# Kernel optimization log

Measured on AMD Instinct MI355X. Metric: run time of the kernel, lower is better.

The kernel has to match this reference:

```python
import jax, jax.numpy as jnp
import numpy as np
from jax import lax

K = 3
ALPHA = 2000.0
TAU = 0.001
MAX_ITER = 100
EPS = 1e-7


def setup_inputs() -> dict:
    key = jax.random.key(0)
    x = jax.random.normal(key, (8, 2048, 32), dtype=jnp.float32)
    return {"x": x}


def _vmd(x):
    B, L, D = x.shape
    # shifted frequency grid, identical across B and D
    f = jnp.fft.fftshift(jnp.fft.fftfreq(L)).astype(x.dtype)          # [L]
    f_bld = f[None, :, None]                                           # [1,L,1]
    # nonnegative-frequency mask; torch code boolean-masks f_shifted >= 0,
    # which is uniform over B and D, so it is a weighted sum over L here
    pos = (f >= 0).astype(x.dtype)[None, None, :, None]                # [1,1,L,1]
    x_hat = jnp.fft.fftshift(jnp.fft.fft(x, axis=1), axes=1)          # [B,L,D] complex

    def step(carry, _):
        u, omega, lam = carry  # u:[B,K,L,D], omega:[B,K,D], lam:[B,L,D]
        # Gauss-Seidel mode updates (each mode sees already-updated others)
        for k_idx in range(K):
            sum_other = jnp.sum(u, axis=1) - u[:, k_idx]               # [B,L,D]
            sum_other_hat = jnp.fft.fftshift(jnp.fft.fft(sum_other, axis=1), axes=1)
            num = x_hat - sum_other_hat + lam * 0.5                    # lam added in freq domain, as in source
            den = 1.0 + 2.0 * ALPHA * (f_bld - omega[:, k_idx][:, None, :]) ** 2
            u_k = jnp.real(jnp.fft.ifft(jnp.fft.ifftshift(num / den, axes=1), axis=1))
            u = u.at[:, k_idx].set(u_k)
        # center-frequency update over nonnegative shifted frequencies
        u_hat = jnp.fft.fftshift(jnp.fft.fft(u, axis=2), axes=2)       # [B,K,L,D]
        p = (u_hat.real ** 2 + u_hat.imag ** 2) * pos                  # |u_hat|^2 masked
        omega = jnp.sum(f[None, None, :, None] * p, axis=2) / (jnp.sum(p, axis=2) + EPS)  # [B,K,D]
        # dual ascent on lambda
        lam = lam + TAU * (x - jnp.sum(u, axis=1))
        return (u, omega, lam), None

    u0 = jnp.zeros((B, K, L, D), x.dtype)
    om0 = jnp.zeros((B, K, D), x.dtype)
    lam0 = jnp.zeros((B, L, D), x.dtype)
    (u, omega, _), _ = lax.scan(jax.checkpoint(step), (u0, om0, lam0), None, length=MAX_ITER)

    # sort modes per batch element by mean center frequency
    order = jnp.argsort(jnp.mean(omega, axis=2), axis=1)               # [B,K]
    u_sorted = jnp.take_along_axis(u, order[:, :, None, None], axis=1)
    return u_sorted[:, 0], u_sorted[:, 1], u_sorted[:, 2]


def reference(x):
    return _vmd(x)
```

## Files before the change

kernel.cpp:

```cpp
#include <hip/hip_runtime.h>

#define PD(i) ((i) + ((i) >> 5))
#define BLD 524288

__device__ __forceinline__ float2 cadd(float2 a, float2 b){ return make_float2(a.x+b.x, a.y+b.y); }
__device__ __forceinline__ float2 csub(float2 a, float2 b){ return make_float2(a.x-b.x, a.y-b.y); }
__device__ __forceinline__ float2 cmul(float2 a, float2 b){ return make_float2(a.x*b.x - a.y*b.y, a.x*b.y + a.y*b.x); }
__device__ __forceinline__ float2 cmuli(float2 a, float s){ return make_float2(-s*a.y, s*a.x); }

template<int CTRL, int RM>
__device__ __forceinline__ float dpp_add(float x){
  int r = __builtin_amdgcn_update_dpp(0, __float_as_int(x), CTRL, RM, 0xf, true);
  return x + __int_as_float(r);
}
__device__ __forceinline__ float wave_sum64(float x){
  x = dpp_add<0x111,0xf>(x);
  x = dpp_add<0x112,0xf>(x);
  x = dpp_add<0x114,0xf>(x);
  x = dpp_add<0x118,0xf>(x);
  x = dpp_add<0x142,0xa>(x);
  x = dpp_add<0x143,0xc>(x);
  return x;
}

template<int SGN>
__device__ __forceinline__ void dft8(float2 a[8]) {
  const float sgn = (float)SGN;
  const float C8 = 0.70710678118654752440f;
  float2 e0=a[0], e1=a[2], e2=a[4], e3=a[6];
  float2 o0=a[1], o1=a[3], o2=a[5], o3=a[7];
  float2 t0=cadd(e0,e2), t1=csub(e0,e2), t2=cadd(e1,e3), t3=csub(e1,e3);
  float2 E0=cadd(t0,t2), E2=csub(t0,t2);
  float2 t3i=cmuli(t3,sgn);
  float2 E1=cadd(t1,t3i), E3=csub(t1,t3i);
  float2 s0=cadd(o0,o2), s1=csub(o0,o2), s2=cadd(o1,o3), s3=csub(o1,o3);
  float2 O0=cadd(s0,s2), O2=csub(s0,s2);
  float2 s3i=cmuli(s3,sgn);
  float2 O1=cadd(s1,s3i), O3=csub(s1,s3i);
  float2 w1o = make_float2(C8*(O1.x - sgn*O1.y), C8*(O1.y + sgn*O1.x));
  float2 w2o = cmuli(O2, sgn);
  float2 w3o = make_float2(-C8*(O3.x + sgn*O3.y), C8*(sgn*O3.x - O3.y));
  a[0]=cadd(E0,O0); a[4]=csub(E0,O0);
  a[1]=cadd(E1,w1o); a[5]=csub(E1,w1o);
  a[2]=cadd(E2,w2o); a[6]=csub(E2,w2o);
  a[3]=cadd(E3,w3o); a[7]=csub(E3,w3o);
}

template<int SGN>
__device__ void fft2048(float2* bufA, float2* bufB, const float2* twd, int tid)
{
  const float sgn = (float)SGN;
  {
    float2 a[8];
    #pragma unroll
    for (int j=0;j<8;j++) a[j] = bufA[PD(tid + 256*j)];
    dft8<SGN>(a);
    float2 tw = twd[tid];
    float2 w1 = make_float2(tw.x, sgn*tw.y), wj = w1;
    #pragma unroll
    for (int j=1;j<8;j++){ a[j] = cmul(a[j], wj); wj = cmul(wj, w1); }
    #pragma unroll
    for (int j=0;j<8;j++) bufB[PD(8*tid + j)] = a[j];
  }
  __syncthreads();
  {
    float2 a[8];
    #pragma unroll
    for (int j=0;j<8;j++) a[j] = bufB[PD(tid + 256*j)];
    dft8<SGN>(a);
    int p = tid >> 3, q = tid & 7;
    float2 tw = twd[p << 3];
    float2 w1 = make_float2(tw.x, sgn*tw.y), wj = w1;
    #pragma unroll
    for (int j=1;j<8;j++){ a[j] = cmul(a[j], wj); wj = cmul(wj, w1); }
    int base = q + (p << 6);
    #pragma unroll
    for (int j=0;j<8;j++) bufA[PD(base + (j<<3))] = a[j];
  }
  __syncthreads();
  {
    float2 a[8];
    #pragma unroll
    for (int j=0;j<8;j++) a[j] = bufA[PD(tid + 256*j)];
    dft8<SGN>(a);
    int p = tid >> 6, q = tid & 63;
    float2 tw = twd[p << 6];
    float2 w1 = make_float2(tw.x, sgn*tw.y), wj = w1;
    #pragma unroll
    for (int j=1;j<8;j++){ a[j] = cmul(a[j], wj); wj = cmul(wj, w1); }
    int base = q + (p << 9);
    #pragma unroll
    for (int j=0;j<8;j++) bufB[PD(base + (j<<6))] = a[j];
  }
  __syncthreads();
  {
    #pragma unroll
    for (int h=0; h<2; h++){
      int q = tid + (h<<8);
      float2 b0 = bufB[PD(q)], b1 = bufB[PD(q+512)], b2 = bufB[PD(q+1024)], b3 = bufB[PD(q+1536)];
      float2 t0=cadd(b0,b2), t1=csub(b0,b2), t2=cadd(b1,b3), t3=csub(b1,b3);
      float2 t3i=cmuli(t3,sgn);
      bufA[PD(q)]      = cadd(t0,t2);
      bufA[PD(q+512)]  = cadd(t1,t3i);
      bufA[PD(q+1024)] = csub(t0,t2);
      bufA[PD(q+1536)] = csub(t1,t3i);
    }
  }
  __syncthreads();
}

__device__ __forceinline__ void dft4p(float2 a[4]){
  float2 t0=cadd(a[0],a[2]), t1=csub(a[0],a[2]), t2=cadd(a[1],a[3]), t3=csub(a[1],a[3]);
  float2 t3i = make_float2(-t3.y, t3.x);
  a[0]=cadd(t0,t2); a[2]=csub(t0,t2);
  a[1]=cadd(t1,t3i); a[3]=csub(t1,t3i);
}

template<bool TRANSP>
__global__ __launch_bounds__(256, 1) void vmd_main(const float* __restrict__ xg,
                                                   float* __restrict__ uout,
                                                   float* __restrict__ omout)
{
  __shared__ float2 sbufA[2112];
  __shared__ float2 sbufB[2112];
  __shared__ float2 stwd[1024];
  __shared__ float  sred[24];

  const int tid = threadIdx.x;
  const int blk = blockIdx.x;
  const int b = blk >> 5;
  const int d = blk & 31;
  const float inv2048 = 1.0f/2048.0f;

  for (int j = tid; j < 1024; j += 256) {
    double th = 3.14159265358979323846 * (double)j / 1024.0;
    stwd[j] = make_float2((float)cos(th), (float)sin(th));
  }

  int idxs[8];
  float fl[4], fh[4];
  #pragma unroll
  for (int c = 0; c < 4; c++) {
    int iL = 4*tid + c;
    idxs[c]   = iL;
    idxs[c+4] = (iL == 0) ? 1024 : (2048 - iL);
    fl[c] = (float)(idxs[c]   - 1024) * inv2048;
    fh[c] = (float)(idxs[c+4] - 1024) * inv2048;
  }
  int sI[8];
  #pragma unroll
  for (int e = 0; e < 8; e++) sI[e] = PD(idxs[e]);

  float xv[8];
  #pragma unroll
  for (int e = 0; e < 8; e++) xv[e] = xg[(b*2048 + idxs[e])*32 + d];

  #pragma unroll
  for (int e = 0; e < 8; e++) {
    float v = (idxs[e] & 1) ? -xv[e] : xv[e];
    sbufA[sI[e]] = make_float2(v, 0.0f);
  }
  __syncthreads();
  fft2048<-1>(sbufA, sbufB, stwd, tid);
  float2 X[8];
  #pragma unroll
  for (int e = 0; e < 8; e++) X[e] = sbufA[sI[e]];

  int rd[4]; float2 wq[4];
  #pragma unroll
  for (int j = 0; j < 4; j++) { int q = tid + 256*j; rd[j] = PD(q); wq[j] = stwd[q]; }
  const int pw0 = PD(4*tid);
  float2 c1w1 = stwd[2*tid];
  float2 c1w2 = cmul(c1w1,c1w1), c1w3 = cmul(c1w2,c1w1);
  float2 s4w1 = stwd[8*(tid>>2)];
  float2 s4w2 = cmul(s4w1,s4w1), s4w3 = cmul(s4w2,s4w1);
  float2 s16w1 = stwd[32*(tid>>4)];
  float2 s16w2 = cmul(s16w1,s16w1), s16w3 = cmul(s16w2,s16w1);
  float2 s64w1 = stwd[128*(tid>>6)];
  float2 s64w2 = cmul(s64w1,s64w1), s64w3 = cmul(s64w2,s64w1);
  int w4i[4], w16i[4], w64i[4];
  { int base = (tid & 3) + ((tid>>2)<<4);
    #pragma unroll
    for (int j=0;j<4;j++) w4i[j]  = PD(base + (j<<2)); }
  { int base = (tid & 15) + ((tid>>4)<<6);
    #pragma unroll
    for (int j=0;j<4;j++) w16i[j] = PD(base + (j<<4)); }
  { int base = (tid & 63) + ((tid>>6)<<8);
    #pragma unroll
    for (int j=0;j<4;j++) w64i[j] = PD(base + (j<<6)); }
  const int zi0 = PD(2*tid), zi1 = PD(2*tid+1);
  const int zi2 = PD((tid==0) ? 512 : (1024 - 2*tid));
  const int zi3 = PD(1023 - 2*tid), zi4 = PD(1022 - 2*tid);

  auto herm = [&]() {
    {
      float2 C[4];
      #pragma unroll
      for (int j=0;j<4;j++){
        float2 lo = sbufB[rd[j]];
        float2 hi = sbufB[rd[j] + 1056];
        float2 Av = cadd(lo,hi), Bv = csub(lo,hi);
        float2 WB = cmul(wq[j], Bv);
        C[j] = make_float2(Av.x - WB.y, Av.y + WB.x);
      }
      dft4p(C);
      C[1]=cmul(C[1],c1w1); C[2]=cmul(C[2],c1w2); C[3]=cmul(C[3],c1w3);
      sbufA[pw0]   = C[0];
      sbufA[pw0+1] = C[1];
      sbufA[pw0+2] = C[2];
      sbufA[pw0+3] = C[3];
    }
    __syncthreads();
    {
      float2 a[4];
      #pragma unroll
      for (int j=0;j<4;j++) a[j] = sbufA[rd[j]];
      dft4p(a);
      a[1]=cmul(a[1],s4w1); a[2]=cmul(a[2],s4w2); a[3]=cmul(a[3],s4w3);
      #pragma unroll
      for (int j=0;j<4;j++) sbufB[w4i[j]] = a[j];
    }
    __syncthreads();
    {
      float2 a[4];
      #pragma unroll
      for (int j=0;j<4;j++) a[j] = sbufB[rd[j]];
      dft4p(a);
      a[1]=cmul(a[1],s16w1); a[2]=cmul(a[2],s16w2); a[3]=cmul(a[3],s16w3);
      #pragma unroll
      for (int j=0;j<4;j++) sbufA[w16i[j]] = a[j];
    }
    __syncthreads();
    {
      float2 a[4];
      #pragma unroll
      for (int j=0;j<4;j++) a[j] = sbufA[rd[j]];
      dft4p(a);
      a[1]=cmul(a[1],s64w1); a[2]=cmul(a[2],s64w2); a[3]=cmul(a[3],s64w3);
      #pragma unroll
      for (int j=0;j<4;j++) sbufB[w64i[j]] = a[j];
    }
    __syncthreads();
    {
      float2 a[4];
      #pragma unroll
      for (int j=0;j<4;j++) a[j] = sbufB[rd[j]];
      dft4p(a);
      #pragma unroll
      for (int j=0;j<4;j++) sbufA[rd[j]] = a[j];
    }
    __syncthreads();
  };

  float2 U[3][8];
  float2 S[8];
  float lam2[8];
  #pragma unroll
  for (int e = 0; e < 8; e++) {
    S[e] = make_float2(0.f, 0.f); lam2[e] = 0.f;
    #pragma unroll
    for (int k = 0; k < 3; k++) U[k][e] = make_float2(0.f, 0.f);
  }
  float om[3] = {0.f, 0.f, 0.f};
  const int wv = tid >> 6, ln = tid & 63;

  for (int iter = 0; iter < 100; iter++) {
    float xl[8];
    #pragma unroll
    for (int e = 0; e < 8; e++) xl[e] = X[e].x + lam2[e];

    float sf[3], sp[3];
    #pragma unroll
    for (int k = 0; k < 3; k++) {
      sf[k] = 0.f; sp[k] = 0.f;
      #pragma unroll
      for (int c = 0; c < 4; c++) {
        float2 numl = make_float2(xl[c]     - S[c].x   + U[k][c].x,
                                  X[c].y    - S[c].y   + U[k][c].y);
        float2 numh = make_float2(xl[c+4]   - S[c+4].x + U[k][c+4].x,
                                  X[c+4].y  - S[c+4].y + U[k][c+4].y);
        float dl = fl[c] - om[k], dh = fh[c] - om[k];
        float rl = __builtin_amdgcn_rcpf(fmaf(4000.0f*dl, dl, 1.0f));
        float rh = __builtin_amdgcn_rcpf(fmaf(4000.0f*dh, dh, 1.0f));
        float2 Vl = make_float2(numl.x*rl, numl.y*rl);
        float2 Vh = make_float2(numh.x*rh, numh.y*rh);
        float2 Ul, Uh;
        if (tid == 0 && c == 0) {
          Ul = make_float2(Vl.x, 0.f);
          Uh = make_float2(Vh.x, 0.f);
        } else {
          Ul = make_float2(0.5f*(Vl.x + Vh.x), 0.5f*(Vl.y - Vh.y));
          Uh = make_float2(Ul.x, -Ul.y);
        }
        S[c].x   += Ul.x - U[k][c].x;   S[c].y   += Ul.y - U[k][c].y;
        S[c+4].x += Uh.x - U[k][c+4].x; S[c+4].y += Uh.y - U[k][c+4].y;
        U[k][c] = Ul; U[k][c+4] = Uh;
        float pw = Uh.x*Uh.x + Uh.y*Uh.y;
        sf[k] = fmaf(fh[c], pw, sf[k]);
        sp[k] += pw;
      }
    }

    #pragma unroll
    for (int e = 0; e < 8; e++) sbufB[sI[e]] = S[e];

    #pragma unroll
    for (int k = 0; k < 3; k++) { sf[k] = wave_sum64(sf[k]); sp[k] = wave_sum64(sp[k]); }
    if (ln == 63) {
      #pragma unroll
      for (int k = 0; k < 3; k++) { sred[wv*6 + k] = sf[k]; sred[wv*6 + 3 + k] = sp[k]; }
    }
    __syncthreads();

    #pragma unroll
    for (int k = 0; k < 3; k++) {
      float a = sred[k] + sred[6+k] + sred[12+k] + sred[18+k];
      float p = sred[3+k] + sred[9+k] + sred[15+k] + sred[21+k];
      om[k] = a * __builtin_amdgcn_rcpf(p + 1e-7f);
    }

    herm();

    {
      float2 z0 = sbufA[zi0];
      float2 z1 = sbufA[zi1];
      float2 h0 = sbufA[zi2];
      float2 h1 = sbufA[zi3];
      float2 h2 = sbufA[zi4];
      float g[8];
      g[0]=z0.x; g[1]=z0.y; g[2]=z1.x; g[3]=z1.y;
      g[4]=h0.x; g[5]=h1.y; g[6]=h1.x; g[7]=h2.y;
      #pragma unroll
      for (int e = 0; e < 8; e++) {
        float sv = g[e] * inv2048;
        if (e & 1) sv = -sv;
        lam2[e] = fmaf(0.0005f, xv[e] - sv, lam2[e]);
      }
    }
  }

  #pragma unroll
  for (int k = 0; k < 3; k++) {
    #pragma unroll
    for (int e = 0; e < 8; e++) sbufB[sI[e]] = U[k][e];
    __syncthreads();
    herm();
    {
      float2 z0 = sbufA[zi0];
      float2 z1 = sbufA[zi1];
      float2 h0 = sbufA[zi2];
      float2 h1 = sbufA[zi3];
      float2 h2 = sbufA[zi4];
      float g[8];
      g[0]=z0.x; g[1]=z0.y; g[2]=z1.x; g[3]=z1.y;
      g[4]=h0.x; g[5]=h1.y; g[6]=h1.x; g[7]=h2.y;
      #pragma unroll
      for (int e = 0; e < 8; e++) {
        float uv = g[e] * inv2048;
        if (e & 1) uv = -uv;
        if (TRANSP) uout[(((size_t)k*8 + b)*32 + d)*2048 + idxs[e]] = uv;
        else        uout[(size_t)k*BLD + ((size_t)b*2048 + idxs[e])*32 + d] = uv;
      }
    }
  }
  if (tid == 0) {
    omout[(b*3 + 0)*32 + d] = om[0];
    omout[(b*3 + 1)*32 + d] = om[1];
    omout[(b*3 + 2)*32 + d] = om[2];
  }
}

__device__ __forceinline__ void order3(const float* sm, int* sord){
  float v0=sm[0], v1=sm[1], v2=sm[2];
  int j0=0,j1=1,j2=2;
  if (v1<v0){float tv=v0;v0=v1;v1=tv;int ti=j0;j0=j1;j1=ti;}
  if (v2<v1){float tv=v1;v1=v2;v2=tv;int ti=j1;j1=j2;j2=ti;}
  if (v1<v0){float tv=v0;v0=v1;v1=tv;int ti=j0;j0=j1;j1=ti;}
  sord[0]=j0; sord[1]=j1; sord[2]=j2;
}

__global__ __launch_bounds__(256) void vmd_permute(const float* __restrict__ wsu,
                                                   const float* __restrict__ omout,
                                                   float* __restrict__ out)
{
  __shared__ float tile[32][33];
  __shared__ float sm[3];
  __shared__ int sord[3];
  int bid = blockIdx.x;
  int lt = bid & 63;
  int b = (bid >> 6) & 7;
  int kpos = bid >> 9;
  int tid = threadIdx.x;
  if (tid < 3) {
    float s = 0.f;
    for (int dd = 0; dd < 32; dd++) s += omout[(b*3 + tid)*32 + dd];
    sm[tid] = s;
  }
  __syncthreads();
  if (tid == 0) order3(sm, sord);
  __syncthreads();
  int ks = sord[kpos];
  int tr = tid >> 5, tc = tid & 31;
  for (int it = 0; it < 4; it++) {
    int dd = tr + it*8;
    tile[dd][tc] = wsu[(((size_t)ks*8 + b)*32 + dd)*2048 + lt*32 + tc];
  }
  __syncthreads();
  for (int it = 0; it < 4; it++) {
    int ll = tr + it*8;
    out[(size_t)kpos*BLD + ((size_t)b*2048 + lt*32 + ll)*32 + tc] = tile[tc][ll];
  }
}

__global__ void vmd_inplace(float* __restrict__ out, const float* __restrict__ omout)
{
  __shared__ float sm[3];
  __shared__ int sord[3];
  int r = blockIdx.x * 256 + threadIdx.x;
  int b = r >> 16;
  if (threadIdx.x < 3) {
    float s = 0.f;
    for (int dd = 0; dd < 32; dd++) s += omout[(b*3 + threadIdx.x)*32 + dd];
    sm[threadIdx.x] = s;
  }
  __syncthreads();
  if (threadIdx.x == 0) order3(sm, sord);
  __syncthreads();
  int o0 = sord[0], o1 = sord[1], o2 = sord[2];
  float v0 = out[(size_t)o0*BLD + r];
  float v1 = out[(size_t)o1*BLD + r];
  float v2 = out[(size_t)o2*BLD + r];
  out[r] = v0;
  out[(size_t)BLD + r] = v1;
  out[(size_t)2*BLD + r] = v2;
}

extern "C" void kernel_launch(void* const* d_in, const int* in_sizes, int n_in,
                              void* d_out, int out_size, void* d_ws, size_t ws_size,
                              hipStream_t stream)
{
  const float* x = (const float*)d_in[0];
  float* out = (float*)d_out;
  const size_t NU = (size_t)3 * BLD;
  size_t need = NU*4 + 768*4;
  if (ws_size >= need) {
    float* wsu  = (float*)d_ws;
    float* wsom = wsu + NU;
    vmd_main<true><<<256, 256, 0, stream>>>(x, wsu, wsom);
    vmd_permute<<<1536, 256, 0, stream>>>(wsu, wsom, out);
  } else {
    float* wsom = (float*)d_ws;
    vmd_main<false><<<256, 256, 0, stream>>>(x, out, wsom);
    vmd_inplace<<<2048, 256, 0, stream>>>(out, wsom);
  }
}
```

Before: 313.2 us.

## Replace shared-memory radix-4 inverse FFT stages with in-wave lane-exchange butterflies

The per-iteration Hermitian inverse FFT used five shared-memory radix-4 passes separated by block barriers. It is replaced by one shared-memory radix-4 pass, followed by six radix-2 stages done inside each wave with ds_bpermute, ds_swizzle and DPP exchanges, and a final 4-way combine read from shared memory. This cuts block-wide barriers per iteration from about five to one or two. The mode update also keeps only half of the spectrum in registers by exploiting conjugate symmetry. The cost is more complex indexing and twiddle setup, extra cross-lane traffic, and some risk of numerical or index errors.

Result: faster. 302.7 us (-3.4%).

```diff
diff --git a/kernel.cpp b/kernel.cpp
--- a/kernel.cpp
+++ b/kernel.cpp
@@ -21,6 +21,24 @@
   x = dpp_add<0x142,0xa>(x);
   x = dpp_add<0x143,0xc>(x);
   return x;
+}
+
+__device__ __forceinline__ float2 exbp(int addr, float2 v){
+  return make_float2(
+    __int_as_float(__builtin_amdgcn_ds_bpermute(addr, __float_as_int(v.x))),
+    __int_as_float(__builtin_amdgcn_ds_bpermute(addr, __float_as_int(v.y))));
+}
+template<int PAT>
+__device__ __forceinline__ float2 exswz(float2 v){
+  return make_float2(
+    __int_as_float(__builtin_amdgcn_ds_swizzle(__float_as_int(v.x), PAT)),
+    __int_as_float(__builtin_amdgcn_ds_swizzle(__float_as_int(v.y), PAT)));
+}
+template<int CTRL>
+__device__ __forceinline__ float2 exdpp(float2 v){
+  return make_float2(
+    __int_as_float(__builtin_amdgcn_update_dpp(0, __float_as_int(v.x), CTRL, 0xF, 0xF, true)),
+    __int_as_float(__builtin_amdgcn_update_dpp(0, __float_as_int(v.y), CTRL, 0xF, 0xF, true)));
 }
 
 template<int SGN>
@@ -126,30 +144,31 @@
   __shared__ float2 stwd[1024];
   __shared__ float  sred[24];
 
-  const int tid = threadIdx.x;
+  float2* sS  = sbufB;
+  float2* sTY = sbufA;
+
+  const int t = threadIdx.x;
+  const int lane = t & 63;
+  const int w = t >> 6;
   const int blk = blockIdx.x;
   const int b = blk >> 5;
   const int d = blk & 31;
   const float inv2048 = 1.0f/2048.0f;
 
-  for (int j = tid; j < 1024; j += 256) {
+  for (int j = t; j < 1024; j += 256) {
     double th = 3.14159265358979323846 * (double)j / 1024.0;
     stwd[j] = make_float2((float)cos(th), (float)sin(th));
   }
 
   int idxs[8];
-  float fl[4], fh[4];
+  float fl[4];
   #pragma unroll
   for (int c = 0; c < 4; c++) {
-    int iL = 4*tid + c;
+    int iL = 4*t + c;
     idxs[c]   = iL;
     idxs[c+4] = (iL == 0) ? 1024 : (2048 - iL);
-    fl[c] = (float)(idxs[c]   - 1024) * inv2048;
-    fh[c] = (float)(idxs[c+4] - 1024) * inv2048;
-  }
-  int sI[8];
-  #pragma unroll
-  for (int e = 0; e < 8; e++) sI[e] = PD(idxs[e]);
+    fl[c] = (float)(iL - 1024) * inv2048;
+  }
 
   float xv[8];
   #pragma unroll
@@ -158,157 +177,191 @@
   #pragma unroll
   for (int e = 0; e < 8; e++) {
     float v = (idxs[e] & 1) ? -xv[e] : xv[e];
-    sbufA[sI[e]] = make_float2(v, 0.0f);
-  }
-  __syncthreads();
-  fft2048<-1>(sbufA, sbufB, stwd, tid);
-  float2 X[8];
-  #pragma unroll
-  for (int e = 0; e < 8; e++) X[e] = sbufA[sI[e]];
-
-  int rd[4]; float2 wq[4];
-  #pragma unroll
-  for (int j = 0; j < 4; j++) { int q = tid + 256*j; rd[j] = PD(q); wq[j] = stwd[q]; }
-  const int pw0 = PD(4*tid);
-  float2 c1w1 = stwd[2*tid];
-  float2 c1w2 = cmul(c1w1,c1w1), c1w3 = cmul(c1w2,c1w1);
-  float2 s4w1 = stwd[8*(tid>>2)];
-  float2 s4w2 = cmul(s4w1,s4w1), s4w3 = cmul(s4w2,s4w1);
-  float2 s16w1 = stwd[32*(tid>>4)];
-  float2 s16w2 = cmul(s16w1,s16w1), s16w3 = cmul(s16w2,s16w1);
-  float2 s64w1 = stwd[128*(tid>>6)];
-  float2 s64w2 = cmul(s64w1,s64w1), s64w3 = cmul(s64w2,s64w1);
-  int w4i[4], w16i[4], w64i[4];
-  { int base = (tid & 3) + ((tid>>2)<<4);
-    #pragma unroll
-    for (int j=0;j<4;j++) w4i[j]  = PD(base + (j<<2)); }
-  { int base = (tid & 15) + ((tid>>4)<<6);
-    #pragma unroll
-    for (int j=0;j<4;j++) w16i[j] = PD(base + (j<<4)); }
-  { int base = (tid & 63) + ((tid>>6)<<8);
-    #pragma unroll
-    for (int j=0;j<4;j++) w64i[j] = PD(base + (j<<6)); }
-  const int zi0 = PD(2*tid), zi1 = PD(2*tid+1);
-  const int zi2 = PD((tid==0) ? 512 : (1024 - 2*tid));
-  const int zi3 = PD(1023 - 2*tid), zi4 = PD(1022 - 2*tid);
-
-  auto herm = [&]() {
-    {
-      float2 C[4];
+    sbufA[PD(idxs[e])] = make_float2(v, 0.0f);
+  }
+  __syncthreads();
+  fft2048<-1>(sbufA, sbufB, stwd, t);
+  float2 X[4];
+  if (t == 0) X[0] = make_float2(sbufA[PD(0)].x, sbufA[PD(1024)].x);
+  else        X[0] = sbufA[PD(4*t)];
+  X[1] = sbufA[PD(4*t+1)];
+  X[2] = sbufA[PD(4*t+2)];
+  X[3] = sbufA[PD(4*t+3)];
+
+  int r6 = ((lane&1)<<5)|((lane&2)<<3)|((lane&4)<<1)|((lane&8)>>1)|((lane&16)>>3)|((lane&32)>>5);
+  const int prb = w*528 + lane;
+  float2 wq[4];
+  #pragma unroll
+  for (int j=0;j<4;j++) wq[j] = stwd[4*lane + 256*j + w];
+  float2 w2561 = stwd[8*lane];
+  float2 w2562 = stwd[16*lane & 2047] ;
+  float2 w2563 = cmul(w2561, w2562);
+  const float sg32 = (lane&32)?-1.f:1.f, sg16 = (lane&16)?-1.f:1.f, sg8 = (lane&8)?-1.f:1.f;
+  const float sg4  = (lane&4) ?-1.f:1.f, sg2  = (lane&2) ?-1.f:1.f, sg1 = (lane&1)?-1.f:1.f;
+  const float2 one = make_float2(1.f, 0.f);
+  float2 tw32 = (lane&32)? stwd[32*(lane&31)]  : one;
+  float2 tw16 = (lane&16)? stwd[64*(lane&15)]  : one;
+  float2 tw8  = (lane&8) ? stwd[128*(lane&7)]  : one;
+  float2 tw4  = (lane&4) ? stwd[256*(lane&3)]  : one;
+  float2 tw2  = (lane&2) ? stwd[512*(lane&1)]  : one;
+  const int bp32 = ((lane^32) << 2);
+  const int tyb = w*264 + r6;
+  float2 tytw[4];
+  #pragma unroll
+  for (int r=0;r<4;r++){
+    int xx2 = 2*w*(r + 4*r6);
+    tytw[r] = (xx2 < 1024) ? stwd[xx2]
+            : make_float2(-stwd[xx2-1024].x, -stwd[xx2-1024].y);
+  }
+  int slA, slB, slC, slD, slE;
+  float2 phA, phB, phC, phD, phE;
+  float s2A, s2B, s2C, s2D, s2E;
+  {
+    int ks[5];
+    ks[0] = 2*t; ks[1] = 2*t+1;
+    ks[2] = (t==0) ? 512 : (1024 - 2*t);
+    ks[3] = 1023 - 2*t; ks[4] = 1022 - 2*t;
+    int   sl[5]; float2 ph[5]; float s2[5];
+    #pragma unroll
+    for (int i=0;i<5;i++){
+      int k1 = ks[i] >> 8, k2 = ks[i] & 255;
+      sl[i] = 66*(k2 & 3) + (k2 >> 2);
+      float2 P = (k1==0)? make_float2(1,0) : (k1==1)? make_float2(0,1)
+               : (k1==2)? make_float2(-1,0) : make_float2(0,-1);
+      ph[i] = P; s2[i] = (k1 & 1) ? -1.f : 1.f;
+    }
+    slA=sl[0]; slB=sl[1]; slC=sl[2]; slD=sl[3]; slE=sl[4];
+    phA=ph[0]; phB=ph[1]; phC=ph[2]; phD=ph[3]; phE=ph[4];
+    s2A=s2[0]; s2B=s2[1]; s2C=s2[2]; s2D=s2[3]; s2E=s2[4];
+  }
+
+  auto stageSpec = [&](float2 v0, float2 v1, float2 v2, float2 v3){
+    if (t == 0) { sS[0] = make_float2(v0.x, 0.f); sS[256] = make_float2(v0.y, 0.f); }
+    else        { sS[t] = v0;                     sS[512 - t] = make_float2(v0.x, -v0.y); }
+    sS[528  + t] = v1;  sS[2095 - t] = make_float2(v1.x, -v1.y);
+    sS[1056 + t] = v2;  sS[1567 - t] = make_float2(v2.x, -v2.y);
+    sS[1584 + t] = v3;  sS[1039 - t] = make_float2(v3.x, -v3.y);
+  };
+
+  auto runFFT = [&](){
+    float2 C[4];
+    #pragma unroll
+    for (int j=0;j<4;j++){
+      float2 lo = sS[prb + 64*j];
+      float2 hi = sS[prb + 64*j + 256];
+      float2 Av = cadd(lo, hi), Bv = csub(lo, hi);
+      float2 WB = cmul(wq[j], Bv);
+      C[j] = make_float2(Av.x - WB.y, Av.y + WB.x);
+    }
+    dft4p(C);
+    C[1] = cmul(C[1], w2561); C[2] = cmul(C[2], w2562); C[3] = cmul(C[3], w2563);
+    #pragma unroll
+    for (int r=0;r<4;r++){
+      float2 e = exbp(bp32, C[r]);
+      C[r] = cmul(make_float2(fmaf(sg32, C[r].x, e.x), fmaf(sg32, C[r].y, e.y)), tw32);
+    }
+    #pragma unroll
+    for (int r=0;r<4;r++){
+      float2 e = exswz<0x401F>(C[r]);
+      C[r] = cmul(make_float2(fmaf(sg16, C[r].x, e.x), fmaf(sg16, C[r].y, e.y)), tw16);
+    }
+    #pragma unroll
+    for (int r=0;r<4;r++){
+      float2 e = exswz<0x201F>(C[r]);
+      C[r] = cmul(make_float2(fmaf(sg8, C[r].x, e.x), fmaf(sg8, C[r].y, e.y)), tw8);
+    }
+    #pragma unroll
+    for (int r=0;r<4;r++){
+      float2 e = exswz<0x101F>(C[r]);
+      C[r] = cmul(make_float2(fmaf(sg4, C[r].x, e.x), fmaf(sg4, C[r].y, e.y)), tw4);
+    }
+    #pragma unroll
+    for (int r=0;r<4;r++){
+      float2 e = exdpp<0x4E>(C[r]);
+      C[r] = cmul(make_float2(fmaf(sg2, C[r].x, e.x), fmaf(sg2, C[r].y, e.y)), tw2);
+    }
+    #pragma unroll
+    for (int r=0;r<4;r++){
+      float2 e = exdpp<0xB1>(C[r]);
+      C[r] = make_float2(fmaf(sg1, C[r].x, e.x), fmaf(sg1, C[r].y, e.y));
+    }
+    #pragma unroll
+    for (int r=0;r<4;r++) sTY[tyb + 66*r] = cmul(C[r], tytw[r]);
+  };
+
+  auto zread = [&](int sl, float2 phi, float s2) -> float2 {
+    float2 a0 = sTY[sl], a1 = sTY[sl+264], a2 = sTY[sl+528], a3 = sTY[sl+792];
+    float ex = fmaf(s2, a2.x, a0.x), ey = fmaf(s2, a2.y, a0.y);
+    float ox = fmaf(s2, a3.x, a1.x), oy = fmaf(s2, a3.y, a1.y);
+    return make_float2(ex + phi.x*ox - phi.y*oy, ey + phi.x*oy + phi.y*ox);
+  };
+
+  float2 U[3][4], S[4];
+  float lam2[8];
+  #pragma unroll
+  for (int c=0;c<4;c++){ S[c] = make_float2(0.f,0.f);
+    #pragma unroll
+    for (int k=0;k<3;k++) U[k][c] = make_float2(0.f,0.f); }
+  #pragma unroll
+  for (int e=0;e<8;e++) lam2[e] = 0.f;
+  float om[3] = {0.f,0.f,0.f};
+
+  for (int iter = 0; iter < 100; ++iter) {
+    float sf[3], sp[3];
+    #pragma unroll
+    for (int k = 0; k < 3; k++) {
+      float omk = om[k];
+      sf[k] = 0.f; sp[k] = 0.f;
+      if (t == 0) {
+        float2 Uo = U[k][0];
+        float n0 = X[0].x + lam2[0] - S[0].x + Uo.x;
+        float n1 = X[0].y + lam2[4] - S[0].y + Uo.y;
+        float d0 = -0.5f - omk, d1 = -omk;
+        float u0 = n0 * __builtin_amdgcn_rcpf(fmaf(4000.f*d0, d0, 1.f));
+        float u1 = n1 * __builtin_amdgcn_rcpf(fmaf(4000.f*d1, d1, 1.f));
+        sp[k] += u1*u1;
+        S[0].x += u0 - Uo.x; S[0].y += u1 - Uo.y;
+        U[k][0] = make_float2(u0, u1);
+      } else {
+        float2 Uo = U[k][0];
+        float bx = X[0].x - S[0].x + Uo.x;
+        float by = X[0].y - S[0].y + Uo.y;
+        float nl = bx + lam2[0], nh = bx + lam2[4];
+        float dl = fl[0] - omk, dh = -fl[0] - omk;
+        float rl = __builtin_amdgcn_rcpf(fmaf(4000.f*dl, dl, 1.f));
+        float rh = __builtin_amdgcn_rcpf(fmaf(4000.f*dh, dh, 1.f));
+        float ux = 0.5f*fmaf(nl, rl, nh*rh);
+        float uy = 0.5f*by*(rl+rh);
+        S[0].x += ux - Uo.x; S[0].y += uy - Uo.y;
+        U[k][0] = make_float2(ux, uy);
+        float pw = fmaf(ux, ux, uy*uy);
+        sf[k] = fmaf(-fl[0], pw, sf[k]); sp[k] += pw;
+      }
       #pragma unroll
-      for (int j=0;j<4;j++){
-        float2 lo = sbufB[rd[j]];
-        float2 hi = sbufB[rd[j] + 1056];
-        float2 Av = cadd(lo,hi), Bv = csub(lo,hi);
-        float2 WB = cmul(wq[j], Bv);
-        C[j] = make_float2(Av.x - WB.y, Av.y + WB.x);
+      for (int c = 1; c < 4; c++) {
+        float2 Uo = U[k][c];
+        float bx = X[c].x - S[c].x + Uo.x;
+        float by = X[c].y - S[c].y + Uo.y;
+        float nl = bx + lam2[c], nh = bx + lam2[4+c];
+        float dl = fl[c] - omk, dh = -fl[c] - omk;
+        float rl = __builtin_amdgcn_rcpf(fmaf(4000.f*dl, dl, 1.f));
+        float rh = __builtin_amdgcn_rcpf(fmaf(4000.f*dh, dh, 1.f));
+        float ux = 0.5f*fmaf(nl, rl, nh*rh);
+        float uy = 0.5f*by*(rl+rh);
+        S[c].x += ux - Uo.x; S[c].y += uy - Uo.y;
+        U[k][c] = make_float2(ux, uy);
+        float pw = fmaf(ux, ux, uy*uy);
+        sf[k] = fmaf(-fl[c], pw, sf[k]); sp[k] += pw;
       }
-      dft4p(C);
-      C[1]=cmul(C[1],c1w1); C[2]=cmul(C[2],c1w2); C[3]=cmul(C[3],c1w3);
-      sbufA[pw0]   = C[0];
-      sbufA[pw0+1] = C[1];
-      sbufA[pw0+2] = C[2];
-      sbufA[pw0+3] = C[3];
-    }
-    __syncthreads();
-    {
-      float2 a[4];
+    }
+
+    stageSpec(S[0], S[1], S[2], S[3]);
+
+    #pragma unroll
+    for (int k = 0; k < 3; k++) { sf[k] = wave_sum64(sf[k]); sp[k] = wave_sum64(sp[k]); }
+    if (lane == 63) {
       #pragma unroll
-      for (int j=0;j<4;j++) a[j] = sbufA[rd[j]];
-      dft4p(a);
-      a[1]=cmul(a[1],s4w1); a[2]=cmul(a[2],s4w2); a[3]=cmul(a[3],s4w3);
-      #pragma unroll
-      for (int j=0;j<4;j++) sbufB[w4i[j]] = a[j];
-    }
-    __syncthreads();
-    {
-      float2 a[4];
-      #pragma unroll
-      for (int j=0;j<4;j++) a[j] = sbufB[rd[j]];
-      dft4p(a);
-      a[1]=cmul(a[1],s16w1); a[2]=cmul(a[2],s16w2); a[3]=cmul(a[3],s16w3);
-      #pragma unroll
-      for (int j=0;j<4;j++) sbufA[w16i[j]] = a[j];
-    }
-    __syncthreads();
-    {
-      float2 a[4];
-      #pragma unroll
-      for (int j=0;j<4;j++) a[j] = sbufA[rd[j]];
-      dft4p(a);
-      a[1]=cmul(a[1],s64w1); a[2]=cmul(a[2],s64w2); a[3]=cmul(a[3],s64w3);
-      #pragma unroll
-      for (int j=0;j<4;j++) sbufB[w64i[j]] = a[j];
-    }
-    __syncthreads();
-    {
-      float2 a[4];
-      #pragma unroll
-      for (int j=0;j<4;j++) a[j] = sbufB[rd[j]];
-      dft4p(a);
-      #pragma unroll
-      for (int j=0;j<4;j++) sbufA[rd[j]] = a[j];
-    }
-    __syncthreads();
-  };
-
-  float2 U[3][8];
-  float2 S[8];
-  float lam2[8];
-  #pragma unroll
-  for (int e = 0; e < 8; e++) {
-    S[e] = make_float2(0.f, 0.f); lam2[e] = 0.f;
-    #pragma unroll
-    for (int k = 0; k < 3; k++) U[k][e] = make_float2(0.f, 0.f);
-  }
-  float om[3] = {0.f, 0.f, 0.f};
-  const int wv = tid >> 6, ln = tid & 63;
-
-  for (int iter = 0; iter < 100; iter++) {
-    float xl[8];
-    #pragma unroll
-    for (int e = 0; e < 8; e++) xl[e] = X[e].x + lam2[e];
-
-    float sf[3], sp[3];
-    #pragma unroll
-    for (int k = 0; k < 3; k++) {
-      sf[k] = 0.f; sp[k] = 0.f;
-      #pragma unroll
-      for (int c = 0; c < 4; c++) {
-        float2 numl = make_float2(xl[c]     - S[c].x   + U[k][c].x,
-                                  X[c].y    - S[c].y   + U[k][c].y);
-        float2 numh = make_float2(xl[c+4]   - S[c+4].x + U[k][c+4].x,
-                                  X[c+4].y  - S[c+4].y + U[k][c+4].y);
-        float dl = fl[c] - om[k], dh = fh[c] - om[k];
-        float rl = __builtin_amdgcn_rcpf(fmaf(4000.0f*dl, dl, 1.0f));
-        float rh = __builtin_amdgcn_rcpf(fmaf(4000.0f*dh, dh, 1.0f));
-        float2 Vl = make_float2(numl.x*rl, numl.y*rl);
-        float2 Vh = make_float2(numh.x*rh, numh.y*rh);
-        float2 Ul, Uh;
-        if (tid == 0 && c == 0) {
-          Ul = make_float2(Vl.x, 0.f);
-          Uh = make_float2(Vh.x, 0.f);
-        } else {
-          Ul = make_float2(0.5f*(Vl.x + Vh.x), 0.5f*(Vl.y - Vh.y));
-          Uh = make_float2(Ul.x, -Ul.y);
-        }
-        S[c].x   += Ul.x - U[k][c].x;   S[c].y   += Ul.y - U[k][c].y;
-        S[c+4].x += Uh.x - U[k][c+4].x; S[c+4].y += Uh.y - U[k][c+4].y;
-        U[k][c] = Ul; U[k][c+4] = Uh;
-        float pw = Uh.x*Uh.x + Uh.y*Uh.y;
-        sf[k] = fmaf(fh[c], pw, sf[k]);
-        sp[k] += pw;
-      }
-    }
-
-    #pragma unroll
-    for (int e = 0; e < 8; e++) sbufB[sI[e]] = S[e];
-
-    #pragma unroll
-    for (int k = 0; k < 3; k++) { sf[k] = wave_sum64(sf[k]); sp[k] = wave_sum64(sp[k]); }
-    if (ln == 63) {
-      #pragma unroll
-      for (int k = 0; k < 3; k++) { sred[wv*6 + k] = sf[k]; sred[wv*6 + 3 + k] = sp[k]; }
+      for (int k = 0; k < 3; k++) { sred[w*6 + k] = sf[k]; sred[w*6 + 3 + k] = sp[k]; }
     }
     __syncthreads();
 
@@ -319,51 +372,50 @@
       om[k] = a * __builtin_amdgcn_rcpf(p + 1e-7f);
     }
 
-    herm();
+    runFFT();
+    __syncthreads();
 
     {
-      float2 z0 = sbufA[zi0];
-      float2 z1 = sbufA[zi1];
-      float2 h0 = sbufA[zi2];
-      float2 h1 = sbufA[zi3];
-      float2 h2 = sbufA[zi4];
+      float2 zA = zread(slA, phA, s2A);
+      float2 zB = zread(slB, phB, s2B);
+      float2 zC = zread(slC, phC, s2C);
+      float2 zD = zread(slD, phD, s2D);
+      float2 zE = zread(slE, phE, s2E);
+      lam2[0] = fmaf(0.0005f, xv[0] - zA.x*inv2048, lam2[0]);
+      lam2[1] = fmaf(0.0005f, xv[1] + zA.y*inv2048, lam2[1]);
+      lam2[2] = fmaf(0.0005f, xv[2] - zB.x*inv2048, lam2[2]);
+      lam2[3] = fmaf(0.0005f, xv[3] + zB.y*inv2048, lam2[3]);
+      lam2[4] = fmaf(0.0005f, xv[4] - zC.x*inv2048, lam2[4]);
+      lam2[5] = fmaf(0.0005f, xv[5] + zD.y*inv2048, lam2[5]);
+      lam2[6] = fmaf(0.0005f, xv[6] - zD.x*inv2048, lam2[6]);
+      lam2[7] = fmaf(0.0005f, xv[7] + zE.y*inv2048, lam2[7]);
+    }
+  }
+
+  #pragma unroll
+  for (int k = 0; k < 3; k++) {
+    stageSpec(U[k][0], U[k][1], U[k][2], U[k][3]);
+    __syncthreads();
+    runFFT();
+    __syncthreads();
+    {
+      float2 zA = zread(slA, phA, s2A);
+      float2 zB = zread(slB, phB, s2B);
+      float2 zC = zread(slC, phC, s2C);
+      float2 zD = zread(slD, phD, s2D);
+      float2 zE = zread(slE, phE, s2E);
       float g[8];
-      g[0]=z0.x; g[1]=z0.y; g[2]=z1.x; g[3]=z1.y;
-      g[4]=h0.x; g[5]=h1.y; g[6]=h1.x; g[7]=h2.y;
-      #pragma unroll
-      for (int e = 0; e < 8; e++) {
-        float sv = g[e] * inv2048;
-        if (e & 1) sv = -sv;
-        lam2[e] = fmaf(0.0005f, xv[e] - sv, lam2[e]);
-      }
-    }
-  }
-
-  #pragma unroll
-  for (int k = 0; k < 3; k++) {
-    #pragma unroll
-    for (int e = 0; e < 8; e++) sbufB[sI[e]] = U[k][e];
-    __syncthreads();
-    herm();
-    {
-      float2 z0 = sbufA[zi0];
-      float2 z1 = sbufA[zi1];
-      float2 h0 = sbufA[zi2];
-      float2 h1 = sbufA[zi3];
-      float2 h2 = sbufA[zi4];
-      float g[8];
-      g[0]=z0.x; g[1]=z0.y; g[2]=z1.x; g[3]=z1.y;
-      g[4]=h0.x; g[5]=h1.y; g[6]=h1.x; g[7]=h2.y;
+      g[0] =  zA.x; g[1] = -zA.y; g[2] =  zB.x; g[3] = -zB.y;
+      g[4] =  zC.x; g[5] = -zD.y; g[6] =  zD.x; g[7] = -zE.y;
       #pragma unroll
       for (int e = 0; e < 8; e++) {
         float uv = g[e] * inv2048;
-        if (e & 1) uv = -uv;
         if (TRANSP) uout[(((size_t)k*8 + b)*32 + d)*2048 + idxs[e]] = uv;
         else        uout[(size_t)k*BLD + ((size_t)b*2048 + idxs[e])*32 + d] = uv;
       }
     }
   }
-  if (tid == 0) {
+  if (t == 0) {
     omout[(b*3 + 0)*32 + d] = om[0];
     omout[(b*3 + 1)*32 + d] = om[1];
     omout[(b*3 + 2)*32 + d] = om[2];
```
